# Kernel optimization log

Measured on AMD Instinct MI355X. Metric: run time of the kernel, lower is better.

The kernel has to match this reference:

```python
import jax, jax.numpy as jnp
import numpy as np

F_IN = 22 * 1000   # flattened EEG trial
D_DENSE = 100      # Dense(100) -> becomes T=100 timesteps of dim 1
H = 128            # LSTM units
N_CLASS = 4


def setup_inputs() -> dict:
    key = jax.random.key(0)
    ks = jax.random.split(key, 8)
    B = 4096
    s1 = 1.0 / np.sqrt(F_IN)
    sr = 1.0 / np.sqrt(H)
    x = jax.random.normal(ks[0], (B, 22, 1000), dtype=jnp.float32)
    W1 = jax.random.uniform(ks[1], (F_IN, D_DENSE), jnp.float32, -s1, s1)
    b1 = jnp.zeros((D_DENSE,), jnp.float32)
    # Keras LSTM kernels: input kernel [1, 4H], recurrent kernel [H, 4H], bias [4H]
    Wk = jax.random.uniform(ks[2], (1, 4 * H), jnp.float32, -1.0, 1.0)
    Wr = jax.random.normal(ks[3], (H, 4 * H), dtype=jnp.float32) * sr
    # Keras unit_forget_bias: f-gate bias initialized to 1
    bl = jnp.concatenate([jnp.zeros(H), jnp.ones(H), jnp.zeros(2 * H)]).astype(jnp.float32)
    W2 = jax.random.uniform(ks[4], (H, N_CLASS), jnp.float32, -sr, sr)
    b2 = jnp.zeros((N_CLASS,), jnp.float32)
    return {"x": x, "W1": W1, "b1": b1, "Wk": Wk, "Wr": Wr, "bl": bl, "W2": W2, "b2": b2}


def _lstm_last(seq, Wk, Wr, bl):
    # seq: [B, T, 1]; returns final hidden state [B, H]
    B = seq.shape[0]
    # precompute input contribution for all steps: [T, B, 4H]
    zx = jnp.einsum('btf,fg->tbg', seq, Wk) + bl

    def step(carry, zxt):
        h, c = carry
        z = zxt + h @ Wr                      # [B, 4H]
        i, f, g, o = jnp.split(z, 4, axis=-1)  # keras gate order: i, f, c, o
        i = jax.nn.sigmoid(i)
        f = jax.nn.sigmoid(f)
        g = jnp.tanh(g)
        o = jax.nn.sigmoid(o)
        c = f * c + i * g
        h = o * jnp.tanh(c)
        return (h, c), None

    init = (jnp.zeros((B, H), seq.dtype), jnp.zeros((B, H), seq.dtype))
    (h, _), _ = jax.lax.scan(step, init, zx)
    return h


def reference(x, W1, b1, Wk, Wr, bl, W2, b2):
    B = x.shape[0]
    flat = x.reshape(B, -1)                 # Flatten
    d = flat @ W1 + b1                      # Dense(100), linear activation
    seq = d.reshape(B, D_DENSE, 1)          # Reshape((100, 1))
    h = _lstm_last(seq, Wk, Wr, bl)         # LSTM(128) -> last hidden state
    logits = h @ W2 + b2                    # Dense(4)
    return jax.nn.softmax(logits, axis=-1)
```

## Files before the change

kernel.cpp:

```cpp
#include <hip/hip_runtime.h>
#include <stdint.h>

#define F_IN   22000
#define B_SZ   4096
#define T_STEPS 100
#define NSPLIT 16
#define NCHUNK 22
#define KSPAN  (NCHUNK * 64)
#define ACC_STRIDE 104
#define ACCB_BYTES ((size_t)B_SZ * ACC_STRIDE * 4)
#define BIMG_BYTES 28672
#define BIMG_HALF  14336
#define W1IMG_BYTES ((size_t)NSPLIT * NCHUNK * BIMG_BYTES)

typedef float f32x4 __attribute__((ext_vector_type(4)));
typedef short s16x8 __attribute__((ext_vector_type(8)));

__device__ inline unsigned short f2bf(float f){
  unsigned u = __builtin_bit_cast(unsigned, f);
  u += 0x7FFFu + ((u >> 16) & 1u);
  return (unsigned short)(u >> 16);
}
__device__ inline float bf2f(unsigned short h){
  return __builtin_bit_cast(float, ((unsigned)h) << 16);
}
__device__ inline float sigf(float x){
  return __builtin_amdgcn_rcpf(1.f + __expf(-x));
}
__device__ inline float tanhf_(float x){
  return 1.f - 2.f * __builtin_amdgcn_rcpf(__expf(2.f * x) + 1.f);
}

__global__ __launch_bounds__(256) void k_zero(float4* __restrict__ p, int n4){
  int i = blockIdx.x * 256 + threadIdx.x;
  if (i < n4) p[i] = make_float4(0.f, 0.f, 0.f, 0.f);
}

__global__ __launch_bounds__(256) void k_w1img(const float* __restrict__ W1,
                                               char* __restrict__ img){
  int ch = blockIdx.x, s = blockIdx.y;
  int k0 = s * KSPAN + ch * 64;
  char* base = img + ((size_t)(s * NCHUNK + ch)) * BIMG_BYTES;
  int tid = threadIdx.x;
  #pragma unroll
  for (int it = 0; it < 4; ++it){
    int task = it * 256 + tid;
    if (task < 896){
      int p  = task * 16;
      int c  = p >> 7;
      int k8 = ((p >> 4) & 7) ^ (c & 7);
      unsigned hw[4], lw[4];
      #pragma unroll
      for (int jj = 0; jj < 4; ++jj){
        float v0 = 0.f, v1 = 0.f;
        int k = k0 + k8 * 8 + jj * 2;
        if (c < 100){
          if (k     < F_IN) v0 = W1[(size_t)k * 100 + c];
          if (k + 1 < F_IN) v1 = W1[(size_t)(k + 1) * 100 + c];
        }
        unsigned short h0 = f2bf(v0), l0 = f2bf(v0 - bf2f(h0));
        unsigned short h1 = f2bf(v1), l1 = f2bf(v1 - bf2f(h1));
        hw[jj] = (unsigned)h0 | ((unsigned)h1 << 16);
        lw[jj] = (unsigned)l0 | ((unsigned)l1 << 16);
      }
      *(uint4*)(base + p)             = make_uint4(hw[0], hw[1], hw[2], hw[3]);
      *(uint4*)(base + BIMG_HALF + p) = make_uint4(lw[0], lw[1], lw[2], lw[3]);
    }
  }
}

__global__ __launch_bounds__(256, 2) void k_dense(const float* __restrict__ x,
                                                  const char* __restrict__ img,
                                                  float* __restrict__ accb){
  __shared__ char Bb0[BIMG_BYTES], Bb1[BIMG_BYTES];
  int tid = threadIdx.x;
  int lane = tid & 63, w = tid >> 6;
  int r = lane & 15, oct = lane >> 4;
  int brow = blockIdx.x * 64;
  int s = blockIdx.y;
  int arow = brow + w * 16 + r;
  const float* xrow = x + (size_t)arow * F_IN;
  const char* isrc = img + (size_t)s * NCHUNK * BIMG_BYTES;
  int kbase = s * KSPAN;

  f32x4 acc[7];
  #pragma unroll
  for (int i = 0; i < 7; ++i) acc[i] = (f32x4)0.f;

  float4 xa0, xa1, xa2, xa3;
  float4 ya0, ya1, ya2, ya3;

#define ALOAD(CH, A0, A1, A2, A3) do{                                        \
    int k0_ = kbase + (CH) * 64;                                             \
    int ka0_ = k0_ + oct * 8;                                                \
    int ka1_ = k0_ + 32 + oct * 8;                                           \
    A0 = make_float4(0.f,0.f,0.f,0.f); A1 = A0; A2 = A0; A3 = A0;            \
    if (ka0_ < F_IN){ A0 = *(const float4*)(xrow + ka0_);                    \
                      A1 = *(const float4*)(xrow + ka0_ + 4); }              \
    if (ka1_ < F_IN){ A2 = *(const float4*)(xrow + ka1_);                    \
                      A3 = *(const float4*)(xrow + ka1_ + 4); }              \
  }while(0)

#define STAGE(CH, BUF) do{                                                   \
    const char* src_ = isrc + (size_t)(CH) * BIMG_BYTES;                     \
    _Pragma("unroll")                                                        \
    for (int i_ = 0; i_ < 7; ++i_){                                          \
      int seg_ = i_ * 4 + w;                                                 \
      __builtin_amdgcn_global_load_lds(                                      \
        (const __attribute__((address_space(1))) void*)(src_ + seg_ * 1024 + lane * 16), \
        (__attribute__((address_space(3))) void*)((BUF) + seg_ * 1024), 16, 0, 0); \
    }                                                                        \
  }while(0)

#define CONVMFMA(BUF, A0, A1, A2, A3) do{                                    \
    float va_[16] = {A0.x,A0.y,A0.z,A0.w, A1.x,A1.y,A1.z,A1.w,               \
                     A2.x,A2.y,A2.z,A2.w, A3.x,A3.y,A3.z,A3.w};              \
    s16x8 ah0_, al0_, ah1_, al1_;                                            \
    _Pragma("unroll")                                                        \
    for (int j_ = 0; j_ < 8; ++j_){                                          \
      unsigned short h_ = f2bf(va_[j_]);                                     \
      ah0_[j_] = (short)h_; al0_[j_] = (short)f2bf(va_[j_] - bf2f(h_));      \
    }                                                                        \
    _Pragma("unroll")                                                        \
    for (int j_ = 0; j_ < 8; ++j_){                                          \
      unsigned short h_ = f2bf(va_[8 + j_]);                                 \
      ah1_[j_] = (short)h_; al1_[j_] = (short)f2bf(va_[8 + j_] - bf2f(h_));  \
    }                                                                        \
    _Pragma("unroll")                                                        \
    for (int ct_ = 0; ct_ < 7; ++ct_){                                       \
      int c_ = ct_ * 16 + r;                                                 \
      int byte0_ = ((c_ * 128 + oct * 16) ^ ((c_ & 7) << 4));                \
      int byte1_ = ((c_ * 128 + 64 + oct * 16) ^ ((c_ & 7) << 4));           \
      s16x8 bh0_ = *(s16x8*)((BUF) + byte0_);                                \
      s16x8 bl0_ = *(s16x8*)((BUF) + BIMG_HALF + byte0_);                    \
      s16x8 bh1_ = *(s16x8*)((BUF) + byte1_);                                \
      s16x8 bl1_ = *(s16x8*)((BUF) + BIMG_HALF + byte1_);                    \
      acc[ct_] = __builtin_amdgcn_mfma_f32_16x16x32_bf16(ah0_, bh0_, acc[ct_], 0, 0, 0); \
      acc[ct_] = __builtin_amdgcn_mfma_f32_16x16x32_bf16(ah0_, bl0_, acc[ct_], 0, 0, 0); \
      acc[ct_] = __builtin_amdgcn_mfma_f32_16x16x32_bf16(al0_, bh0_, acc[ct_], 0, 0, 0); \
      acc[ct_] = __builtin_amdgcn_mfma_f32_16x16x32_bf16(ah1_, bh1_, acc[ct_], 0, 0, 0); \
      acc[ct_] = __builtin_amdgcn_mfma_f32_16x16x32_bf16(ah1_, bl1_, acc[ct_], 0, 0, 0); \
      acc[ct_] = __builtin_amdgcn_mfma_f32_16x16x32_bf16(al1_, bh1_, acc[ct_], 0, 0, 0); \
    }                                                                        \
  }while(0)

  STAGE(0, Bb0);
  ALOAD(0, xa0, xa1, xa2, xa3);
  __syncthreads();

  for (int ch = 0; ch < NCHUNK; ch += 2){
    if (ch + 1 < NCHUNK){
      STAGE(ch + 1, Bb1);
      ALOAD(ch + 1, ya0, ya1, ya2, ya3);
    }
    CONVMFMA(Bb0, xa0, xa1, xa2, xa3);
    __syncthreads();
    if (ch + 1 < NCHUNK){
      if (ch + 2 < NCHUNK){
        STAGE(ch + 2, Bb0);
        ALOAD(ch + 2, xa0, xa1, xa2, xa3);
      }
      CONVMFMA(Bb1, ya0, ya1, ya2, ya3);
      __syncthreads();
    }
  }

#undef ALOAD
#undef STAGE
#undef CONVMFMA

  #pragma unroll
  for (int ct = 0; ct < 7; ++ct){
    int col = ct * 16 + r;
    if (col < 100){
      #pragma unroll
      for (int reg = 0; reg < 4; ++reg){
        int orow = brow + w * 16 + oct * 4 + reg;
        atomicAdd(&accb[(size_t)orow * ACC_STRIDE + col], acc[ct][reg]);
      }
    }
  }
}

__global__ __launch_bounds__(256, 1) void k_lstm(const float* __restrict__ accb,
                                                 const float* __restrict__ b1,
                                                 const float* __restrict__ Wk,
                                                 const float* __restrict__ Wr,
                                                 const float* __restrict__ bl,
                                                 const float* __restrict__ W2,
                                                 const float* __restrict__ b2,
                                                 float* __restrict__ out){
  __shared__ unsigned short hbuf[2][16 * 128];
  __shared__ float dld[16][ACC_STRIDE];
  __shared__ float hf[16][132];
  int tid = threadIdx.x;
  int lane = tid & 63, w = tid >> 6;
  int oct = lane >> 4, lr = lane & 15;
  int brow = blockIdx.x * 16;

  for (int i = tid; i < 2048; i += 256) hbuf[0][i] = 0;
  for (int i = tid; i < 16 * T_STEPS; i += 256){
    int r = i / T_STEPS, t = i % T_STEPS;
    dld[r][t] = accb[(size_t)(brow + r) * ACC_STRIDE + t] + b1[t];
  }

  float wkv[4][2], blv[4][2];
  s16x8 bfrag[4][2][4];
  #pragma unroll
  for (int G = 0; G < 4; ++G){
    #pragma unroll
    for (int tt = 0; tt < 2; ++tt){
      int col = G * 128 + w * 32 + tt * 16 + lr;
      wkv[G][tt] = Wk[col];
      blv[G][tt] = bl[col];
      #pragma unroll
      for (int kk = 0; kk < 4; ++kk){
        s16x8 f;
        #pragma unroll
        for (int j = 0; j < 8; ++j){
          int k = kk * 32 + oct * 8 + j;
          f[j] = (short)f2bf(Wr[(size_t)k * 512 + col]);
        }
        bfrag[G][tt][kk] = f;
      }
    }
  }
  float cst[2][4];
  #pragma unroll
  for (int tt = 0; tt < 2; ++tt)
    #pragma unroll
    for (int reg = 0; reg < 4; ++reg) cst[tt][reg] = 0.f;
  __syncthreads();

  for (int t = 0; t < T_STEPS; ++t){
    int cur = t & 1;
    f32x4 acc[4][2];
    float dv[4];
    #pragma unroll
    for (int reg = 0; reg < 4; ++reg) dv[reg] = dld[oct * 4 + reg][t];
    #pragma unroll
    for (int G = 0; G < 4; ++G)
      #pragma unroll
      for (int tt = 0; tt < 2; ++tt)
        #pragma unroll
        for (int reg = 0; reg < 4; ++reg)
          acc[G][tt][reg] = dv[reg] * wkv[G][tt] + blv[G][tt];
    #pragma unroll
    for (int kk = 0; kk < 4; ++kk){
      int abyte = (lr * 256 + kk * 64 + oct * 16) ^ ((lr & 7) << 4);
      s16x8 a = *(s16x8*)((char*)hbuf[cur] + abyte);
      #pragma unroll
      for (int G = 0; G < 4; ++G)
        #pragma unroll
        for (int tt = 0; tt < 2; ++tt)
          acc[G][tt] = __builtin_amdgcn_mfma_f32_16x16x32_bf16(a, bfrag[G][tt][kk], acc[G][tt], 0, 0, 0);
    }
    #pragma unroll
    for (int tt = 0; tt < 2; ++tt){
      #pragma unroll
      for (int reg = 0; reg < 4; ++reg){
        float iv = sigf(acc[0][tt][reg]);
        float fv = sigf(acc[1][tt][reg]);
        float gv = tanhf_(acc[2][tt][reg]);
        float ov = sigf(acc[3][tt][reg]);
        float cv = fv * cst[tt][reg] + iv * gv;
        cst[tt][reg] = cv;
        float hv = ov * tanhf_(cv);
        int row = oct * 4 + reg;
        int col = w * 32 + tt * 16 + lr;
        int byte = (row * 256 + col * 2) ^ ((row & 7) << 4);
        *(unsigned short*)((char*)hbuf[cur ^ 1] + byte) = f2bf(hv);
        if (t == T_STEPS - 1) hf[row][col] = hv;
      }
    }
    __syncthreads();
  }

  if (tid < 64){
    int row = tid >> 2, cl = tid & 3;
    float a = b2[cl];
    #pragma unroll 8
    for (int j = 0; j < 128; ++j) a += hf[row][j] * W2[j * 4 + cl];
    float m = fmaxf(a, __shfl_xor(a, 1));
    m = fmaxf(m, __shfl_xor(m, 2));
    float e = __expf(a - m);
    float se = e + __shfl_xor(e, 1);
    se += __shfl_xor(se, 2);
    out[(size_t)(brow + row) * 4 + cl] = e * __builtin_amdgcn_rcpf(se);
  }
}

extern "C" void kernel_launch(void* const* d_in, const int* in_sizes, int n_in,
                              void* d_out, int out_size, void* d_ws, size_t ws_size,
                              hipStream_t stream){
  const float* x  = (const float*)d_in[0];
  const float* W1 = (const float*)d_in[1];
  const float* b1 = (const float*)d_in[2];
  const float* Wk = (const float*)d_in[3];
  const float* Wr = (const float*)d_in[4];
  const float* bl = (const float*)d_in[5];
  const float* W2 = (const float*)d_in[6];
  const float* b2 = (const float*)d_in[7];
  float* out = (float*)d_out;

  float* accb = (float*)d_ws;
  char*  img  = (char*)d_ws + ACCB_BYTES;
  const int n4 = B_SZ * ACC_STRIDE / 4;

  k_zero<<<(n4 + 255) / 256, 256, 0, stream>>>((float4*)accb, n4);
  k_w1img<<<dim3(NCHUNK, NSPLIT), 256, 0, stream>>>(W1, img);
  k_dense<<<dim3(B_SZ / 64, NSPLIT), 256, 0, stream>>>(x, img, accb);
  k_lstm<<<B_SZ / 16, 256, 0, stream>>>(accb, b1, Wk, Wr, bl, W2, b2, out);
}
```

Before: 262.2 us.

## Widen LSTM blocks to 8 waves, prepack Wr fragments, stage W1 tile in LDS

```diff
diff --git a/kernel.cpp b/kernel.cpp
--- a/kernel.cpp
+++ b/kernel.cpp
@@ -12,6 +12,7 @@
 #define BIMG_BYTES 28672
 #define BIMG_HALF  14336
 #define W1IMG_BYTES ((size_t)NSPLIT * NCHUNK * BIMG_BYTES)
+#define WRIMG_BYTES (128 * 1024)
 
 typedef float f32x4 __attribute__((ext_vector_type(4)));
 typedef short s16x8 __attribute__((ext_vector_type(8)));
@@ -38,13 +39,21 @@
 
 __global__ __launch_bounds__(256) void k_w1img(const float* __restrict__ W1,
                                                char* __restrict__ img){
+  __shared__ float tile[64][129];
   int ch = blockIdx.x, s = blockIdx.y;
   int k0 = s * KSPAN + ch * 64;
   char* base = img + ((size_t)(s * NCHUNK + ch)) * BIMG_BYTES;
   int tid = threadIdx.x;
-  #pragma unroll
-  for (int it = 0; it < 4; ++it){
-    int task = it * 256 + tid;
+  for (int idx = tid; idx < 64 * 128; idx += 256){
+    int k = idx >> 7, c = idx & 127;
+    float v = 0.f;
+    if (c < 100 && (k0 + k) < F_IN) v = W1[(size_t)(k0 + k) * 100 + c];
+    tile[k][c] = v;
+  }
+  __syncthreads();
+  #pragma unroll
+  for (int q = 0; q < 4; ++q){
+    int task = q * 256 + tid;
     if (task < 896){
       int p  = task * 16;
       int c  = p >> 7;
@@ -52,12 +61,8 @@
       unsigned hw[4], lw[4];
       #pragma unroll
       for (int jj = 0; jj < 4; ++jj){
-        float v0 = 0.f, v1 = 0.f;
-        int k = k0 + k8 * 8 + jj * 2;
-        if (c < 100){
-          if (k     < F_IN) v0 = W1[(size_t)k * 100 + c];
-          if (k + 1 < F_IN) v1 = W1[(size_t)(k + 1) * 100 + c];
-        }
+        float v0 = tile[k8 * 8 + jj * 2][c];
+        float v1 = tile[k8 * 8 + jj * 2 + 1][c];
         unsigned short h0 = f2bf(v0), l0 = f2bf(v0 - bf2f(h0));
         unsigned short h1 = f2bf(v1), l1 = f2bf(v1 - bf2f(h1));
         hw[jj] = (unsigned)h0 | ((unsigned)h1 << 16);
@@ -67,6 +72,23 @@
       *(uint4*)(base + BIMG_HALF + p) = make_uint4(lw[0], lw[1], lw[2], lw[3]);
     }
   }
+}
+
+__global__ __launch_bounds__(256) void k_wrimg(const float* __restrict__ Wr,
+                                               char* __restrict__ wrimg){
+  int gid = blockIdx.x * 256 + threadIdx.x;
+  int lane = gid & 63, slot = gid >> 6;
+  int kk = slot & 3, G = (slot >> 2) & 3, w = slot >> 4;
+  int oct = lane >> 4, lr = lane & 15;
+  int col = G * 128 + w * 16 + lr;
+  unsigned pk[4];
+  #pragma unroll
+  for (int jj = 0; jj < 4; ++jj){
+    float v0 = Wr[(size_t)(kk * 32 + oct * 8 + jj * 2)     * 512 + col];
+    float v1 = Wr[(size_t)(kk * 32 + oct * 8 + jj * 2 + 1) * 512 + col];
+    pk[jj] = (unsigned)f2bf(v0) | ((unsigned)f2bf(v1) << 16);
+  }
+  *(uint4*)(wrimg + (size_t)gid * 16) = make_uint4(pk[0], pk[1], pk[2], pk[3]);
 }
 
 __global__ __launch_bounds__(256, 2) void k_dense(const float* __restrict__ x,
@@ -182,10 +204,10 @@
   }
 }
 
-__global__ __launch_bounds__(256, 1) void k_lstm(const float* __restrict__ accb,
+__global__ __launch_bounds__(512, 2) void k_lstm(const float* __restrict__ accb,
                                                  const float* __restrict__ b1,
                                                  const float* __restrict__ Wk,
-                                                 const float* __restrict__ Wr,
+                                                 const char* __restrict__ wrimg,
                                                  const float* __restrict__ bl,
                                                  const float* __restrict__ W2,
                                                  const float* __restrict__ b2,
@@ -198,80 +220,63 @@
   int oct = lane >> 4, lr = lane & 15;
   int brow = blockIdx.x * 16;
 
-  for (int i = tid; i < 2048; i += 256) hbuf[0][i] = 0;
-  for (int i = tid; i < 16 * T_STEPS; i += 256){
+  for (int i = tid; i < 2048; i += 512) hbuf[0][i] = 0;
+  for (int i = tid; i < 16 * T_STEPS; i += 512){
     int r = i / T_STEPS, t = i % T_STEPS;
     dld[r][t] = accb[(size_t)(brow + r) * ACC_STRIDE + t] + b1[t];
   }
 
-  float wkv[4][2], blv[4][2];
-  s16x8 bfrag[4][2][4];
+  float wkv[4], blv[4];
+  s16x8 bfrag[4][4];
   #pragma unroll
   for (int G = 0; G < 4; ++G){
-    #pragma unroll
-    for (int tt = 0; tt < 2; ++tt){
-      int col = G * 128 + w * 32 + tt * 16 + lr;
-      wkv[G][tt] = Wk[col];
-      blv[G][tt] = bl[col];
-      #pragma unroll
-      for (int kk = 0; kk < 4; ++kk){
-        s16x8 f;
-        #pragma unroll
-        for (int j = 0; j < 8; ++j){
-          int k = kk * 32 + oct * 8 + j;
-          f[j] = (short)f2bf(Wr[(size_t)k * 512 + col]);
-        }
-        bfrag[G][tt][kk] = f;
-      }
-    }
-  }
-  float cst[2][4];
-  #pragma unroll
-  for (int tt = 0; tt < 2; ++tt)
-    #pragma unroll
-    for (int reg = 0; reg < 4; ++reg) cst[tt][reg] = 0.f;
+    int col = G * 128 + w * 16 + lr;
+    wkv[G] = Wk[col];
+    blv[G] = bl[col];
+    #pragma unroll
+    for (int kk = 0; kk < 4; ++kk){
+      bfrag[G][kk] = *(const s16x8*)(wrimg +
+          ((size_t)(((w * 4 + G) * 4 + kk) * 64 + lane)) * 16);
+    }
+  }
+  float cst[4];
+  #pragma unroll
+  for (int reg = 0; reg < 4; ++reg) cst[reg] = 0.f;
   __syncthreads();
 
   for (int t = 0; t < T_STEPS; ++t){
     int cur = t & 1;
-    f32x4 acc[4][2];
+    f32x4 acc[4];
     float dv[4];
     #pragma unroll
     for (int reg = 0; reg < 4; ++reg) dv[reg] = dld[oct * 4 + reg][t];
     #pragma unroll
     for (int G = 0; G < 4; ++G)
       #pragma unroll
-      for (int tt = 0; tt < 2; ++tt)
-        #pragma unroll
-        for (int reg = 0; reg < 4; ++reg)
-          acc[G][tt][reg] = dv[reg] * wkv[G][tt] + blv[G][tt];
+      for (int reg = 0; reg < 4; ++reg)
+        acc[G][reg] = dv[reg] * wkv[G] + blv[G];
     #pragma unroll
     for (int kk = 0; kk < 4; ++kk){
       int abyte = (lr * 256 + kk * 64 + oct * 16) ^ ((lr & 7) << 4);
       s16x8 a = *(s16x8*)((char*)hbuf[cur] + abyte);
       #pragma unroll
       for (int G = 0; G < 4; ++G)
-        #pragma unroll
-        for (int tt = 0; tt < 2; ++tt)
-          acc[G][tt] = __builtin_amdgcn_mfma_f32_16x16x32_bf16(a, bfrag[G][tt][kk], acc[G][tt], 0, 0, 0);
-    }
-    #pragma unroll
-    for (int tt = 0; tt < 2; ++tt){
-      #pragma unroll
-      for (int reg = 0; reg < 4; ++reg){
-        float iv = sigf(acc[0][tt][reg]);
-        float fv = sigf(acc[1][tt][reg]);
-        float gv = tanhf_(acc[2][tt][reg]);
-        float ov = sigf(acc[3][tt][reg]);
-        float cv = fv * cst[tt][reg] + iv * gv;
-        cst[tt][reg] = cv;
-        float hv = ov * tanhf_(cv);
-        int row = oct * 4 + reg;
-        int col = w * 32 + tt * 16 + lr;
-        int byte = (row * 256 + col * 2) ^ ((row & 7) << 4);
-        *(unsigned short*)((char*)hbuf[cur ^ 1] + byte) = f2bf(hv);
-        if (t == T_STEPS - 1) hf[row][col] = hv;
-      }
+        acc[G] = __builtin_amdgcn_mfma_f32_16x16x32_bf16(a, bfrag[G][kk], acc[G], 0, 0, 0);
+    }
+    #pragma unroll
+    for (int reg = 0; reg < 4; ++reg){
+      float iv = sigf(acc[0][reg]);
+      float fv = sigf(acc[1][reg]);
+      float gv = tanhf_(acc[2][reg]);
+      float ov = sigf(acc[3][reg]);
+      float cv = fv * cst[reg] + iv * gv;
+      cst[reg] = cv;
+      float hv = ov * tanhf_(cv);
+      int row = oct * 4 + reg;
+      int col = w * 16 + lr;
+      int byte = (row * 256 + col * 2) ^ ((row & 7) << 4);
+      *(unsigned short*)((char*)hbuf[cur ^ 1] + byte) = f2bf(hv);
+      if (t == T_STEPS - 1) hf[row][col] = hv;
     }
     __syncthreads();
   }
@@ -303,12 +308,14 @@
   const float* b2 = (const float*)d_in[7];
   float* out = (float*)d_out;
 
-  float* accb = (float*)d_ws;
-  char*  img  = (char*)d_ws + ACCB_BYTES;
+  float* accb  = (float*)d_ws;
+  char*  img   = (char*)d_ws + ACCB_BYTES;
+  char*  wrimg = (char*)d_ws + ACCB_BYTES + W1IMG_BYTES;
   const int n4 = B_SZ * ACC_STRIDE / 4;
 
   k_zero<<<(n4 + 255) / 256, 256, 0, stream>>>((float4*)accb, n4);
   k_w1img<<<dim3(NCHUNK, NSPLIT), 256, 0, stream>>>(W1, img);
+  k_wrimg<<<32, 256, 0, stream>>>(Wr, wrimg);
   k_dense<<<dim3(B_SZ / 64, NSPLIT), 256, 0, stream>>>(x, img, accb);
-  k_lstm<<<B_SZ / 16, 256, 0, stream>>>(accb, b1, Wk, Wr, bl, W2, b2, out);
-}
+  k_lstm<<<B_SZ / 16, 512, 0, stream>>>(accb, b1, Wk, wrimg, bl, W2, b2, out);
+}
```

Result: faster. 242.9 us (-7.4%).
